# Kernel optimization log

Hardware: AMD Instinct MI355X
Metric: run time of the kernel (lower is better)

## Reference

```python
import jax, jax.numpy as jnp
import numpy as np

NUM_HEADS = 16
HIDDEN = 1024
HEAD_DIM = HIDDEN // NUM_HEADS


def setup_inputs() -> dict:
    key = jax.random.key(0)
    ks = jax.random.split(key, 12)
    B, S, H = 4, 1024, HIDDEN
    s = 1.0 / np.sqrt(H)
    inp = {
        "aspect_hidden": jax.random.normal(ks[0], (B, S, H), jnp.float32),
        "opinion_hidden": jax.random.normal(ks[1], (B, S, H), jnp.float32),
        "attention_mask": jnp.ones((B, S), jnp.int32),
        # torch nn.Linear weights are [out, in]
        "Wq": jax.random.normal(ks[2], (H, H), jnp.float32) * s,
        "bq": jnp.zeros((H,), jnp.float32),
        "Wk": jax.random.normal(ks[3], (H, H), jnp.float32) * s,
        "bk": jnp.zeros((H,), jnp.float32),
        "Wv": jax.random.normal(ks[4], (H, H), jnp.float32) * s,
        "bv": jnp.zeros((H,), jnp.float32),
        "Wo": jax.random.normal(ks[5], (H, H), jnp.float32) * s,
        "bo": jnp.zeros((H,), jnp.float32),
        # nn.Bilinear(H, H, 1): weight [1, H, H], bias [1]
        "Wbil": jax.random.normal(ks[6], (1, H, H), jnp.float32) * s,
        "bbil": jnp.zeros((1,), jnp.float32),
    }
    return inp


def reference(aspect_hidden, opinion_hidden, attention_mask,
              Wq, bq, Wk, bk, Wv, bv, Wo, bo, Wbil, bbil):
    B, Sq, H = aspect_hidden.shape
    Sk = opinion_hidden.shape[1]
    nh, hd = NUM_HEADS, HEAD_DIM
    scale = hd ** (-0.5)

    q = (aspect_hidden @ Wq.T + bq).reshape(B, Sq, nh, hd).transpose(0, 2, 1, 3)
    k = (opinion_hidden @ Wk.T + bk).reshape(B, Sk, nh, hd).transpose(0, 2, 1, 3)
    v = (opinion_hidden @ Wv.T + bv).reshape(B, Sk, nh, hd).transpose(0, 2, 1, 3)

    # bilinear span bias: span[b,s] = a[b,s] @ Wbil[0] @ o[b,s] + bbil
    span = jnp.einsum('bsh,hk,bsk->bs', aspect_hidden, Wbil[0], opinion_hidden) + bbil[0]

    # scores [B, nh, Sq, Sk] with span bias broadcast over heads and keys
    scores = jnp.einsum('bhqd,bhkd->bhqk', q, k) * scale + span[:, None, :, None]
    scores = jnp.where(attention_mask[:, None, None, :] == 0, -jnp.inf, scores)

    probs = jax.nn.softmax(scores, axis=-1)
    ctx = jnp.einsum('bhqk,bhkd->bhqd', probs, v)
    ctx = ctx.transpose(0, 2, 1, 3).reshape(B, Sq, H)
    return ctx @ Wo.T + bo
```

## Files before the change

kernel.cpp:

```cpp
#include <hip/hip_runtime.h>
#include <hip/hip_bf16.h>
#include <stdint.h>

typedef __attribute__((ext_vector_type(4))) float f32x4;
typedef __attribute__((ext_vector_type(16))) float f32x16;
typedef __attribute__((ext_vector_type(8))) short bf16x8;
typedef __attribute__((ext_vector_type(4))) unsigned int u32x4;
typedef unsigned short u16;

#define GBL_AS1(p) ((const __attribute__((address_space(1))) void*)(p))
#define LDS_AS3(p) ((__attribute__((address_space(3))) void*)(p))

static __device__ __forceinline__ u16 f2bf(float f) {
  __hip_bfloat16 h = __float2bfloat16(f);
  union { __hip_bfloat16 h; u16 u; } c; c.h = h;
  return c.u;
}

__global__ __launch_bounds__(256) void cast_f32_bf16(const float* __restrict__ src,
                                                     u16* __restrict__ dst, int n4) {
  int i = blockIdx.x * blockDim.x + threadIdx.x;
  if (i >= n4) return;
  float4 v = reinterpret_cast<const float4*>(src)[i];
  ushort4 o;
  o.x = f2bf(v.x); o.y = f2bf(v.y); o.z = f2bf(v.z); o.w = f2bf(v.w);
  reinterpret_cast<ushort4*>(dst)[i] = o;
}

static __device__ __forceinline__ void gemm_core(const u16* __restrict__ Atile,
                                                 const u16* __restrict__ Btile,
                                                 u16* lds_a, u16* lds_b,
                                                 f32x4 acc[4][4]) {
  const int tid = threadIdx.x;
  const int lane = tid & 63;
  const int wv = tid >> 6;
  const int wm = wv >> 1, wn = wv & 1;
  const int fr = lane & 15, fq = lane >> 4;
  for (int kt = 0; kt < 32; ++kt) {
#pragma unroll
    for (int i = 0; i < 2; ++i) {
      const int cb = (wv * 2 + i) * 64;
      const int c = cb + lane;
      const int row = c >> 2;
      const int off = (c & 3) * 8;
      __builtin_amdgcn_global_load_lds(GBL_AS1(Atile + (size_t)row * 1024 + kt * 32 + off),
                                       LDS_AS3(lds_a + cb * 8), 16, 0, 0);
      __builtin_amdgcn_global_load_lds(GBL_AS1(Btile + (size_t)row * 1024 + kt * 32 + off),
                                       LDS_AS3(lds_b + cb * 8), 16, 0, 0);
    }
    __syncthreads();
    bf16x8 af[4], bfv[4];
#pragma unroll
    for (int mi = 0; mi < 4; ++mi)
      af[mi] = *(const bf16x8*)&lds_a[(wm * 64 + mi * 16 + fr) * 32 + fq * 8];
#pragma unroll
    for (int ni = 0; ni < 4; ++ni)
      bfv[ni] = *(const bf16x8*)&lds_b[(wn * 64 + ni * 16 + fr) * 32 + fq * 8];
#pragma unroll
    for (int mi = 0; mi < 4; ++mi)
#pragma unroll
      for (int ni = 0; ni < 4; ++ni)
        acc[mi][ni] = __builtin_amdgcn_mfma_f32_16x16x32_bf16(af[mi], bfv[ni], acc[mi][ni], 0, 0, 0);
    __syncthreads();
  }
}

__global__ __launch_bounds__(256) void qkv_gemm(
    const u16* __restrict__ aB, const u16* __restrict__ oB,
    const u16* __restrict__ Wq, const u16* __restrict__ Wk, const u16* __restrict__ Wv,
    const float* __restrict__ bq, const float* __restrict__ bk, const float* __restrict__ bv,
    u16* __restrict__ q_ws, u16* __restrict__ k_ws, u16* __restrict__ vt_ws) {
  __shared__ __align__(16) u16 lds_a[128 * 32];
  __shared__ __align__(16) u16 lds_b[128 * 32];
  const int mt = blockIdx.x;
  const int nt = blockIdx.y;
  const int w = nt >> 3, ntl = nt & 7;
  const u16* A = (w == 0) ? aB : oB;
  const u16* W = (w == 0) ? Wq : (w == 1) ? Wk : Wv;
  const float* bias = (w == 0) ? bq : (w == 1) ? bk : bv;
  f32x4 acc[4][4];
#pragma unroll
  for (int i = 0; i < 4; ++i)
#pragma unroll
    for (int j = 0; j < 4; ++j) acc[i][j] = (f32x4){0.f, 0.f, 0.f, 0.f};
  gemm_core(A + (size_t)mt * 128 * 1024, W + (size_t)ntl * 128 * 1024, lds_a, lds_b, acc);
  const int lane = threadIdx.x & 63, wvi = threadIdx.x >> 6;
  const int wm = wvi >> 1, wn = wvi & 1, fr = lane & 15, fq = lane >> 4;
  u16* dst01 = (w == 0) ? q_ws : k_ws;
#pragma unroll
  for (int mi = 0; mi < 4; ++mi)
#pragma unroll
    for (int ni = 0; ni < 4; ++ni)
#pragma unroll
      for (int r = 0; r < 4; ++r) {
        int m = mt * 128 + wm * 64 + mi * 16 + fq * 4 + r;
        int nl = ntl * 128 + wn * 64 + ni * 16 + fr;
        float v = acc[mi][ni][r] + bias[nl];
        int b = m >> 10, s = m & 1023, h = nl >> 6, d = nl & 63;
        u16 u = f2bf(v);
        if (w < 2) dst01[(((size_t)(b * 16 + h)) * 1024 + s) * 64 + d] = u;
        else       vt_ws[(((size_t)(b * 16 + h)) * 64 + d) * 1024 + s] = u;
      }
}

__global__ __launch_bounds__(256, 2) void attn_kernel(
    const u16* __restrict__ q_ws, const u16* __restrict__ k_ws,
    const u16* __restrict__ vt_ws, const int* __restrict__ mask,
    u16* __restrict__ ctx_ws) {
  __shared__ __align__(16) u16 k_lds[2][128 * 64];
  __shared__ __align__(16) u16 vt_lds[2][64 * 128];
  __shared__ __align__(16) float mb_lds[2][128];
  __shared__ __align__(16) float scl_lds[4][32];
  const int bid = blockIdx.x;
  const int bh = bid & 63, qt = bid >> 6;
  const int b = bh >> 4, h = bh & 15;
  const int tid = threadIdx.x, lane = tid & 63, wv = tid >> 6;
  const int l31 = lane & 31, hi = lane >> 5;
  const u16* qbase = q_ws + (size_t)bh * 65536 + (size_t)qt * 8192;
  const u16* kbase = k_ws + (size_t)bh * 65536;
  const u16* vtbase = vt_ws + (size_t)bh * 65536;
  const int* maskb = mask + b * 1024;
  const float SCL2 = 0.18033688f;

#define STAGE_KV(kt_, buf_) do { \
    _Pragma("unroll") \
    for (int i_ = 0; i_ < 4; ++i_) { \
      int cb_ = (wv * 4 + i_) * 64; \
      int c_ = cb_ + lane; \
      int rK_ = c_ >> 3, cK_ = c_ & 7; \
      __builtin_amdgcn_global_load_lds(GBL_AS1(kbase + (size_t)((kt_) * 128 + rK_) * 64 + ((cK_ ^ (rK_ & 7)) * 8)), \
                                       LDS_AS3(&k_lds[buf_][cb_ * 8]), 16, 0, 0); \
      int rV_ = c_ >> 4, cV_ = c_ & 15; \
      __builtin_amdgcn_global_load_lds(GBL_AS1(vtbase + (size_t)rV_ * 1024 + (kt_) * 128 + ((cV_ ^ (rV_ & 15)) * 8)), \
                                       LDS_AS3(&vt_lds[buf_][cb_ * 8]), 16, 0, 0); \
    } \
    if (tid < 128) mb_lds[buf_][tid] = maskb[(kt_) * 128 + tid] ? 0.0f : -30000.0f; \
  } while (0)

#pragma unroll
  for (int i_ = 0; i_ < 4; ++i_) {
    int cb_ = (wv * 4 + i_) * 64;
    int c_ = cb_ + lane;
    int rQ = c_ >> 3, cQ = c_ & 7;
    __builtin_amdgcn_global_load_lds(GBL_AS1(qbase + (size_t)rQ * 64 + ((cQ ^ (rQ & 7)) * 8)),
                                     LDS_AS3(&k_lds[1][cb_ * 8]), 16, 0, 0);
  }
  if (tid < 128) mb_lds[0][tid] = maskb[tid] ? 0.0f : -30000.0f;
  __syncthreads();
  bf16x8 qf[4];
  {
    int rq = wv * 32 + l31;
    const u16* qr = &k_lds[1][rq * 64];
    int rx = rq & 7;
#pragma unroll
    for (int ds = 0; ds < 4; ++ds)
      qf[ds] = *(const bf16x8*)&qr[((ds * 2 + hi) ^ rx) * 8];
  }
  __syncthreads();
  STAGE_KV(0, 0);
  __syncthreads();

  f32x16 ctx0, ctx1;
#pragma unroll
  for (int z = 0; z < 16; ++z) { ctx0[z] = 0.f; ctx1[z] = 0.f; }
  float mrow = -1e30f, lrow = 0.f;

  for (int kt = 0; kt < 8; ++kt) {
    const int cur = kt & 1;
    if (kt < 7) STAGE_KV(kt + 1, (kt + 1) & 1);

    f32x16 sc[4];
#pragma unroll
    for (int kb = 0; kb < 4; ++kb) {
      f32x16 a;
#pragma unroll
      for (int z = 0; z < 16; ++z) a[z] = 0.f;
      int r = kb * 32 + l31;
      const u16* kr = &k_lds[cur][r * 64];
      int rx = r & 7;
#pragma unroll
      for (int ds = 0; ds < 4; ++ds) {
        bf16x8 kf = *(const bf16x8*)&kr[((ds * 2 + hi) ^ rx) * 8];
        a = __builtin_amdgcn_mfma_f32_32x32x16_bf16(kf, qf[ds], a, 0, 0, 0);
      }
      sc[kb] = a;
    }

    float pmax = -3.0e38f;
#pragma unroll
    for (int kb = 0; kb < 4; ++kb)
#pragma unroll
      for (int g = 0; g < 4; ++g) {
        float4 mb = *(const float4*)&mb_lds[cur][kb * 32 + g * 8 + hi * 4];
        const float* mbp = (const float*)&mb;
#pragma unroll
        for (int i2 = 0; i2 < 4; ++i2) {
          float v = fmaf(sc[kb][g * 4 + i2], SCL2, mbp[i2]);
          sc[kb][g * 4 + i2] = v;
          pmax = fmaxf(pmax, v);
        }
      }
    pmax = fmaxf(pmax, __shfl_xor(pmax, 32));

    if (__any(pmax > mrow + 8.0f)) {
      float mnew = fmaxf(mrow, pmax);
      float scl = __builtin_exp2f(mrow - mnew);
      mrow = mnew;
      lrow *= scl;
      if (hi == 0) scl_lds[wv][l31] = scl;
      asm volatile("s_waitcnt lgkmcnt(0)" ::: "memory");
#pragma unroll
      for (int g = 0; g < 4; ++g) {
        float4 s4 = *(const float4*)&scl_lds[wv][g * 8 + hi * 4];
        const float* sp = (const float*)&s4;
#pragma unroll
        for (int i2 = 0; i2 < 4; ++i2) {
          ctx0[g * 4 + i2] *= sp[i2];
          ctx1[g * 4 + i2] *= sp[i2];
        }
      }
    }

    float psum = 0.f;
#pragma unroll
    for (int kb = 0; kb < 4; ++kb)
#pragma unroll
      for (int r2 = 0; r2 < 16; ++r2) {
        float p = __builtin_exp2f(sc[kb][r2] - mrow);
        sc[kb][r2] = p;
        psum += p;
      }
    psum += __shfl_xor(psum, 32);
    lrow += psum;

#pragma unroll
    for (int kb = 0; kb < 4; ++kb) {
      unsigned int w[8];
#pragma unroll
      for (int j = 0; j < 8; ++j) {
        unsigned int t;
        asm("v_cvt_pk_bf16_f32 %0, %1, %2" : "=v"(t) : "v"(sc[kb][2 * j]), "v"(sc[kb][2 * j + 1]));
        w[j] = t;
      }
      unsigned int sw0 = (unsigned)__shfl_xor((int)w[0], 32), sw1 = (unsigned)__shfl_xor((int)w[1], 32);
      unsigned int sw2 = (unsigned)__shfl_xor((int)w[2], 32), sw3 = (unsigned)__shfl_xor((int)w[3], 32);
      unsigned int sw4 = (unsigned)__shfl_xor((int)w[4], 32), sw5 = (unsigned)__shfl_xor((int)w[5], 32);
      unsigned int sw6 = (unsigned)__shfl_xor((int)w[6], 32), sw7 = (unsigned)__shfl_xor((int)w[7], 32);
      union { u32x4 u; bf16x8 b; } P0, P1;
      P0.u = (u32x4){ hi ? sw2 : w[0], hi ? sw3 : w[1], hi ? w[2] : sw0, hi ? w[3] : sw1 };
      P1.u = (u32x4){ hi ? sw6 : w[4], hi ? sw7 : w[5], hi ? w[6] : sw4, hi ? w[7] : sw5 };
#pragma unroll
      for (int db = 0; db < 2; ++db) {
        int rv = db * 32 + l31;
        const u16* vr = &vt_lds[cur][rv * 128];
        int rvx = rv & 15;
        bf16x8 v0 = *(const bf16x8*)&vr[((kb * 4 + hi) ^ rvx) * 8];
        bf16x8 v1 = *(const bf16x8*)&vr[((kb * 4 + 2 + hi) ^ rvx) * 8];
        if (db == 0) {
          ctx0 = __builtin_amdgcn_mfma_f32_32x32x16_bf16(P0.b, v0, ctx0, 0, 0, 0);
          ctx0 = __builtin_amdgcn_mfma_f32_32x32x16_bf16(P1.b, v1, ctx0, 0, 0, 0);
        } else {
          ctx1 = __builtin_amdgcn_mfma_f32_32x32x16_bf16(P0.b, v0, ctx1, 0, 0, 0);
          ctx1 = __builtin_amdgcn_mfma_f32_32x32x16_bf16(P1.b, v1, ctx1, 0, 0, 0);
        }
      }
    }
    __syncthreads();
  }

  float inv = (lrow > 0.f) ? 1.0f / lrow : 0.f;
  if (hi == 0) scl_lds[wv][l31] = inv;
  asm volatile("s_waitcnt lgkmcnt(0)" ::: "memory");
  const int sbase = qt * 128 + wv * 32;
#pragma unroll
  for (int g = 0; g < 4; ++g) {
    float4 s4 = *(const float4*)&scl_lds[wv][g * 8 + hi * 4];
    const float* sp = (const float*)&s4;
#pragma unroll
    for (int i2 = 0; i2 < 4; ++i2) {
      int s = sbase + g * 8 + hi * 4 + i2;
      size_t rowoff = ((size_t)(b * 1024 + s)) * 1024 + h * 64;
      ctx_ws[rowoff + l31]      = f2bf(ctx0[g * 4 + i2] * sp[i2]);
      ctx_ws[rowoff + 32 + l31] = f2bf(ctx1[g * 4 + i2] * sp[i2]);
    }
  }
#undef STAGE_KV
}

__global__ __launch_bounds__(256) void out_gemm(const u16* __restrict__ ctxB,
                                                const u16* __restrict__ Wo,
                                                const float* __restrict__ bo,
                                                float* __restrict__ out) {
  __shared__ __align__(16) u16 lds_a[128 * 32];
  __shared__ __align__(16) u16 lds_b[128 * 32];
  const int mt = blockIdx.x, nt = blockIdx.y;
  f32x4 acc[4][4];
#pragma unroll
  for (int i = 0; i < 4; ++i)
#pragma unroll
    for (int j = 0; j < 4; ++j) acc[i][j] = (f32x4){0.f, 0.f, 0.f, 0.f};
  gemm_core(ctxB + (size_t)mt * 128 * 1024, Wo + (size_t)nt * 128 * 1024, lds_a, lds_b, acc);
  const int lane = threadIdx.x & 63, wvi = threadIdx.x >> 6;
  const int wm = wvi >> 1, wn = wvi & 1, fr = lane & 15, fq = lane >> 4;
#pragma unroll
  for (int mi = 0; mi < 4; ++mi)
#pragma unroll
    for (int ni = 0; ni < 4; ++ni)
#pragma unroll
      for (int r = 0; r < 4; ++r) {
        int m = mt * 128 + wm * 64 + mi * 16 + fq * 4 + r;
        int n = nt * 128 + wn * 64 + ni * 16 + fr;
        out[(size_t)m * 1024 + n] = acc[mi][ni][r] + bo[n];
      }
}

extern "C" void kernel_launch(void* const* d_in, const int* in_sizes, int n_in,
                              void* d_out, int out_size, void* d_ws, size_t ws_size,
                              hipStream_t stream) {
  const float* aspect = (const float*)d_in[0];
  const float* opinion = (const float*)d_in[1];
  const int* mask = (const int*)d_in[2];
  const float* Wq = (const float*)d_in[3];
  const float* bq = (const float*)d_in[4];
  const float* Wk = (const float*)d_in[5];
  const float* bk = (const float*)d_in[6];
  const float* Wv = (const float*)d_in[7];
  const float* bv = (const float*)d_in[8];
  const float* Wo = (const float*)d_in[9];
  const float* bo = (const float*)d_in[10];
  float* out = (float*)d_out;
  char* ws = (char*)d_ws;

  const size_t MB = 1u << 20;
  u16* aB    = (u16*)(ws + 0 * MB);
  u16* oB    = (u16*)(ws + 8 * MB);
  u16* WqB   = (u16*)(ws + 16 * MB);
  u16* WkB   = (u16*)(ws + 18 * MB);
  u16* WvB   = (u16*)(ws + 20 * MB);
  u16* WoB   = (u16*)(ws + 22 * MB);
  u16* q_ws  = (u16*)(ws + 24 * MB);
  u16* k_ws  = (u16*)(ws + 32 * MB);
  u16* vt_ws = (u16*)(ws + 40 * MB);
  u16* ctx_ws= (u16*)(ws + 48 * MB);

  cast_f32_bf16<<<4096, 256, 0, stream>>>(aspect, aB, 1048576);
  cast_f32_bf16<<<4096, 256, 0, stream>>>(opinion, oB, 1048576);
  cast_f32_bf16<<<1024, 256, 0, stream>>>(Wq, WqB, 262144);
  cast_f32_bf16<<<1024, 256, 0, stream>>>(Wk, WkB, 262144);
  cast_f32_bf16<<<1024, 256, 0, stream>>>(Wv, WvB, 262144);
  cast_f32_bf16<<<1024, 256, 0, stream>>>(Wo, WoB, 262144);
  qkv_gemm<<<dim3(32, 24), 256, 0, stream>>>(aB, oB, WqB, WkB, WvB, bq, bk, bv,
                                             q_ws, k_ws, vt_ws);
  attn_kernel<<<512, 256, 0, stream>>>(q_ws, k_ws, vt_ws, mask, ctx_ws);
  out_gemm<<<dim3(32, 8), 256, 0, stream>>>(ctx_ws, WoB, bo, out);
}
```

Before: 124.0 us.

## Fuse casts, double-buffer swizzled GEMMs, shrink attention key tiles, precompute mask flags

Replaces the six cast launches with one fused cast kernel, which also records per-64-key mask flags. The shared GEMM core moves to K=64 tiles with XOR-swizzled LDS and double buffering, so global loads overlap the MFMA work. The softmax scale is folded into Q at the QKV epilogue. Attention now uses 64-key tiles with smaller LDS to allow occupancy 4, and applies the mask only in tiles whose flag is set. The flags live in the tail of the output buffer, which out_gemm later overwrites; this relies on out_size being an element count and on kernel ordering.

```diff
diff --git a/kernel.cpp b/kernel.cpp
--- a/kernel.cpp
+++ b/kernel.cpp
@@ -17,61 +17,100 @@
   return c.u;
 }
 
-__global__ __launch_bounds__(256) void cast_f32_bf16(const float* __restrict__ src,
-                                                     u16* __restrict__ dst, int n4) {
-  int i = blockIdx.x * blockDim.x + threadIdx.x;
-  if (i >= n4) return;
-  float4 v = reinterpret_cast<const float4*>(src)[i];
-  ushort4 o;
-  o.x = f2bf(v.x); o.y = f2bf(v.y); o.z = f2bf(v.z); o.w = f2bf(v.w);
-  reinterpret_cast<ushort4*>(dst)[i] = o;
-}
-
-static __device__ __forceinline__ void gemm_core(const u16* __restrict__ Atile,
-                                                 const u16* __restrict__ Btile,
-                                                 u16* lds_a, u16* lds_b,
-                                                 f32x4 acc[4][4]) {
-  const int tid = threadIdx.x;
-  const int lane = tid & 63;
-  const int wv = tid >> 6;
+__global__ __launch_bounds__(256) void fused_cast(
+    const float* __restrict__ a, const float* __restrict__ o,
+    const float* __restrict__ wq_, const float* __restrict__ wk_,
+    const float* __restrict__ wv_, const float* __restrict__ wo_,
+    const int* __restrict__ mask,
+    u16* __restrict__ aB, u16* __restrict__ oB,
+    u16* __restrict__ WqB, u16* __restrict__ WkB,
+    u16* __restrict__ WvB, u16* __restrict__ WoB,
+    int* __restrict__ flags) {
+  if (blockIdx.x == 0 && threadIdx.x < 64) {
+    int bb = threadIdx.x >> 4, kt = threadIdx.x & 15;
+    int anyz = 0;
+    for (int s = 0; s < 64; ++s) anyz |= (mask[bb * 1024 + kt * 64 + s] == 0);
+    flags[threadIdx.x] = anyz;
+  }
+  int idx = blockIdx.x * 256 + threadIdx.x;
+#pragma unroll
+  for (int j = 0; j < 4; ++j) {
+    int i = idx + j * 786432;
+    const float* src; u16* dst; int off;
+    if (i < 1048576) { src = a; dst = aB; off = i; }
+    else if (i < 2097152) { src = o; dst = oB; off = i - 1048576; }
+    else {
+      int w = (i - 2097152) >> 18; off = (i - 2097152) & 262143;
+      src = (w == 0) ? wq_ : (w == 1) ? wk_ : (w == 2) ? wv_ : wo_;
+      dst = (w == 0) ? WqB : (w == 1) ? WkB : (w == 2) ? WvB : WoB;
+    }
+    float4 v = reinterpret_cast<const float4*>(src)[off];
+    ushort4 ov;
+    ov.x = f2bf(v.x); ov.y = f2bf(v.y); ov.z = f2bf(v.z); ov.w = f2bf(v.w);
+    reinterpret_cast<ushort4*>(dst)[off] = ov;
+  }
+}
+
+static __device__ __forceinline__ void gemm_core2(const u16* __restrict__ A,
+                                                  const u16* __restrict__ B,
+                                                  u16* lds_a, u16* lds_b,
+                                                  f32x4 acc[4][4]) {
+  const int tid = threadIdx.x, lane = tid & 63, wv = tid >> 6;
   const int wm = wv >> 1, wn = wv & 1;
   const int fr = lane & 15, fq = lane >> 4;
-  for (int kt = 0; kt < 32; ++kt) {
-#pragma unroll
-    for (int i = 0; i < 2; ++i) {
-      const int cb = (wv * 2 + i) * 64;
-      const int c = cb + lane;
-      const int row = c >> 2;
-      const int off = (c & 3) * 8;
-      __builtin_amdgcn_global_load_lds(GBL_AS1(Atile + (size_t)row * 1024 + kt * 32 + off),
-                                       LDS_AS3(lds_a + cb * 8), 16, 0, 0);
-      __builtin_amdgcn_global_load_lds(GBL_AS1(Btile + (size_t)row * 1024 + kt * 32 + off),
-                                       LDS_AS3(lds_b + cb * 8), 16, 0, 0);
+
+#define GSTAGE(kt_, buf_) do { \
+    _Pragma("unroll") \
+    for (int i_ = 0; i_ < 4; ++i_) { \
+      int cb_ = (wv * 4 + i_) * 64; \
+      int c_ = cb_ + lane; \
+      int r_ = c_ >> 3; \
+      int sc_ = ((c_ & 7) ^ (r_ & 7)) * 8; \
+      __builtin_amdgcn_global_load_lds(GBL_AS1(A + (size_t)r_ * 1024 + (kt_) * 64 + sc_), \
+                                       LDS_AS3(lds_a + (buf_) * 8192 + cb_ * 8), 16, 0, 0); \
+      __builtin_amdgcn_global_load_lds(GBL_AS1(B + (size_t)r_ * 1024 + (kt_) * 64 + sc_), \
+                                       LDS_AS3(lds_b + (buf_) * 8192 + cb_ * 8), 16, 0, 0); \
+    } \
+  } while (0)
+
+  GSTAGE(0, 0);
+  __syncthreads();
+  for (int kt = 0; kt < 16; ++kt) {
+    const int cur = kt & 1;
+    if (kt < 15) GSTAGE(kt + 1, cur ^ 1);
+    const u16* la = lds_a + cur * 8192;
+    const u16* lb = lds_b + cur * 8192;
+#pragma unroll
+    for (int ks = 0; ks < 2; ++ks) {
+      bf16x8 af[4], bfv[4];
+#pragma unroll
+      for (int mi = 0; mi < 4; ++mi) {
+        int r = wm * 64 + mi * 16 + fr;
+        af[mi] = *(const bf16x8*)&la[r * 64 + (((ks * 4 + fq) ^ (r & 7)) * 8)];
+      }
+#pragma unroll
+      for (int ni = 0; ni < 4; ++ni) {
+        int r = wn * 64 + ni * 16 + fr;
+        bfv[ni] = *(const bf16x8*)&lb[r * 64 + (((ks * 4 + fq) ^ (r & 7)) * 8)];
+      }
+#pragma unroll
+      for (int mi = 0; mi < 4; ++mi)
+#pragma unroll
+        for (int ni = 0; ni < 4; ++ni)
+          acc[mi][ni] = __builtin_amdgcn_mfma_f32_16x16x32_bf16(af[mi], bfv[ni], acc[mi][ni], 0, 0, 0);
     }
     __syncthreads();
-    bf16x8 af[4], bfv[4];
-#pragma unroll
-    for (int mi = 0; mi < 4; ++mi)
-      af[mi] = *(const bf16x8*)&lds_a[(wm * 64 + mi * 16 + fr) * 32 + fq * 8];
-#pragma unroll
-    for (int ni = 0; ni < 4; ++ni)
-      bfv[ni] = *(const bf16x8*)&lds_b[(wn * 64 + ni * 16 + fr) * 32 + fq * 8];
-#pragma unroll
-    for (int mi = 0; mi < 4; ++mi)
-#pragma unroll
-      for (int ni = 0; ni < 4; ++ni)
-        acc[mi][ni] = __builtin_amdgcn_mfma_f32_16x16x32_bf16(af[mi], bfv[ni], acc[mi][ni], 0, 0, 0);
-    __syncthreads();
-  }
-}
-
-__global__ __launch_bounds__(256) void qkv_gemm(
+  }
+#undef GSTAGE
+}
+
+__global__ __launch_bounds__(256, 2) void qkv_gemm(
     const u16* __restrict__ aB, const u16* __restrict__ oB,
     const u16* __restrict__ Wq, const u16* __restrict__ Wk, const u16* __restrict__ Wv,
     const float* __restrict__ bq, const float* __restrict__ bk, const float* __restrict__ bv,
     u16* __restrict__ q_ws, u16* __restrict__ k_ws, u16* __restrict__ vt_ws) {
-  __shared__ __align__(16) u16 lds_a[128 * 32];
-  __shared__ __align__(16) u16 lds_b[128 * 32];
+  __shared__ __align__(16) u16 lds_a[2 * 128 * 64];
+  __shared__ __align__(16) u16 lds_b[2 * 128 * 64];
   const int mt = blockIdx.x;
   const int nt = blockIdx.y;
   const int w = nt >> 3, ntl = nt & 7;
@@ -83,10 +122,11 @@
   for (int i = 0; i < 4; ++i)
 #pragma unroll
     for (int j = 0; j < 4; ++j) acc[i][j] = (f32x4){0.f, 0.f, 0.f, 0.f};
-  gemm_core(A + (size_t)mt * 128 * 1024, W + (size_t)ntl * 128 * 1024, lds_a, lds_b, acc);
+  gemm_core2(A + (size_t)mt * 128 * 1024, W + (size_t)ntl * 128 * 1024, lds_a, lds_b, acc);
   const int lane = threadIdx.x & 63, wvi = threadIdx.x >> 6;
   const int wm = wvi >> 1, wn = wvi & 1, fr = lane & 15, fq = lane >> 4;
   u16* dst01 = (w == 0) ? q_ws : k_ws;
+  const float qscl = (w == 0) ? 0.18033688f : 1.0f;
 #pragma unroll
   for (int mi = 0; mi < 4; ++mi)
 #pragma unroll
@@ -95,7 +135,7 @@
       for (int r = 0; r < 4; ++r) {
         int m = mt * 128 + wm * 64 + mi * 16 + fq * 4 + r;
         int nl = ntl * 128 + wn * 64 + ni * 16 + fr;
-        float v = acc[mi][ni][r] + bias[nl];
+        float v = (acc[mi][ni][r] + bias[nl]) * qscl;
         int b = m >> 10, s = m & 1023, h = nl >> 6, d = nl & 63;
         u16 u = f2bf(v);
         if (w < 2) dst01[(((size_t)(b * 16 + h)) * 1024 + s) * 64 + d] = u;
@@ -103,13 +143,12 @@
       }
 }
 
-__global__ __launch_bounds__(256, 2) void attn_kernel(
+__global__ __launch_bounds__(256, 4) void attn_kernel(
     const u16* __restrict__ q_ws, const u16* __restrict__ k_ws,
     const u16* __restrict__ vt_ws, const int* __restrict__ mask,
-    u16* __restrict__ ctx_ws) {
-  __shared__ __align__(16) u16 k_lds[2][128 * 64];
-  __shared__ __align__(16) u16 vt_lds[2][64 * 128];
-  __shared__ __align__(16) float mb_lds[2][128];
+    const int* __restrict__ flags, u16* __restrict__ ctx_ws) {
+  __shared__ __align__(16) u16 k_lds[2][64 * 64];
+  __shared__ __align__(16) u16 vt_lds[2][64 * 64];
   __shared__ __align__(16) float scl_lds[4][32];
   const int bid = blockIdx.x;
   const int bh = bid & 63, qt = bid >> 6;
@@ -119,38 +158,38 @@
   const u16* qbase = q_ws + (size_t)bh * 65536 + (size_t)qt * 8192;
   const u16* kbase = k_ws + (size_t)bh * 65536;
   const u16* vtbase = vt_ws + (size_t)bh * 65536;
-  const int* maskb = mask + b * 1024;
-  const float SCL2 = 0.18033688f;
 
 #define STAGE_KV(kt_, buf_) do { \
     _Pragma("unroll") \
-    for (int i_ = 0; i_ < 4; ++i_) { \
-      int cb_ = (wv * 4 + i_) * 64; \
+    for (int i_ = 0; i_ < 2; ++i_) { \
+      int cb_ = (wv * 2 + i_) * 64; \
       int c_ = cb_ + lane; \
-      int rK_ = c_ >> 3, cK_ = c_ & 7; \
-      __builtin_amdgcn_global_load_lds(GBL_AS1(kbase + (size_t)((kt_) * 128 + rK_) * 64 + ((cK_ ^ (rK_ & 7)) * 8)), \
+      int r_ = c_ >> 3; \
+      int sc_ = ((c_ & 7) ^ (r_ & 7)) * 8; \
+      __builtin_amdgcn_global_load_lds(GBL_AS1(kbase + (size_t)((kt_) * 64 + r_) * 64 + sc_), \
                                        LDS_AS3(&k_lds[buf_][cb_ * 8]), 16, 0, 0); \
-      int rV_ = c_ >> 4, cV_ = c_ & 15; \
-      __builtin_amdgcn_global_load_lds(GBL_AS1(vtbase + (size_t)rV_ * 1024 + (kt_) * 128 + ((cV_ ^ (rV_ & 15)) * 8)), \
+      __builtin_amdgcn_global_load_lds(GBL_AS1(vtbase + (size_t)r_ * 1024 + (kt_) * 64 + sc_), \
                                        LDS_AS3(&vt_lds[buf_][cb_ * 8]), 16, 0, 0); \
     } \
-    if (tid < 128) mb_lds[buf_][tid] = maskb[(kt_) * 128 + tid] ? 0.0f : -30000.0f; \
   } while (0)
 
-#pragma unroll
-  for (int i_ = 0; i_ < 4; ++i_) {
-    int cb_ = (wv * 4 + i_) * 64;
-    int c_ = cb_ + lane;
-    int rQ = c_ >> 3, cQ = c_ & 7;
-    __builtin_amdgcn_global_load_lds(GBL_AS1(qbase + (size_t)rQ * 64 + ((cQ ^ (rQ & 7)) * 8)),
-                                     LDS_AS3(&k_lds[1][cb_ * 8]), 16, 0, 0);
-  }
-  if (tid < 128) mb_lds[0][tid] = maskb[tid] ? 0.0f : -30000.0f;
+  {
+    u16* qstage = &k_lds[0][0];
+#pragma unroll
+    for (int i_ = 0; i_ < 4; ++i_) {
+      int cb_ = (wv * 4 + i_) * 64;
+      int c_ = cb_ + lane;
+      int r_ = c_ >> 3;
+      int sc_ = ((c_ & 7) ^ (r_ & 7)) * 8;
+      __builtin_amdgcn_global_load_lds(GBL_AS1(qbase + (size_t)r_ * 64 + sc_),
+                                       LDS_AS3(qstage + cb_ * 8), 16, 0, 0);
+    }
+  }
   __syncthreads();
   bf16x8 qf[4];
   {
     int rq = wv * 32 + l31;
-    const u16* qr = &k_lds[1][rq * 64];
+    const u16* qr = &k_lds[0][0] + rq * 64;
     int rx = rq & 7;
 #pragma unroll
     for (int ds = 0; ds < 4; ++ds)
@@ -165,13 +204,13 @@
   for (int z = 0; z < 16; ++z) { ctx0[z] = 0.f; ctx1[z] = 0.f; }
   float mrow = -1e30f, lrow = 0.f;
 
-  for (int kt = 0; kt < 8; ++kt) {
+  for (int kt = 0; kt < 16; ++kt) {
     const int cur = kt & 1;
-    if (kt < 7) STAGE_KV(kt + 1, (kt + 1) & 1);
-
-    f32x16 sc[4];
-#pragma unroll
-    for (int kb = 0; kb < 4; ++kb) {
+    if (kt < 15) STAGE_KV(kt + 1, cur ^ 1);
+
+    f32x16 sc[2];
+#pragma unroll
+    for (int kb = 0; kb < 2; ++kb) {
       f32x16 a;
 #pragma unroll
       for (int z = 0; z < 16; ++z) a[z] = 0.f;
@@ -186,20 +225,21 @@
       sc[kb] = a;
     }
 
+    if (flags[b * 16 + kt]) {
+#pragma unroll
+      for (int kb = 0; kb < 2; ++kb)
+#pragma unroll
+        for (int r2 = 0; r2 < 16; ++r2) {
+          int key = kb * 32 + (r2 & 3) + 8 * (r2 >> 2) + 4 * hi;
+          if (mask[b * 1024 + kt * 64 + key] == 0) sc[kb][r2] = -30000.0f;
+        }
+    }
+
     float pmax = -3.0e38f;
 #pragma unroll
-    for (int kb = 0; kb < 4; ++kb)
-#pragma unroll
-      for (int g = 0; g < 4; ++g) {
-        float4 mb = *(const float4*)&mb_lds[cur][kb * 32 + g * 8 + hi * 4];
-        const float* mbp = (const float*)&mb;
-#pragma unroll
-        for (int i2 = 0; i2 < 4; ++i2) {
-          float v = fmaf(sc[kb][g * 4 + i2], SCL2, mbp[i2]);
-          sc[kb][g * 4 + i2] = v;
-          pmax = fmaxf(pmax, v);
-        }
-      }
+    for (int kb = 0; kb < 2; ++kb)
+#pragma unroll
+      for (int r2 = 0; r2 < 16; ++r2) pmax = fmaxf(pmax, sc[kb][r2]);
     pmax = fmaxf(pmax, __shfl_xor(pmax, 32));
 
     if (__any(pmax > mrow + 8.0f)) {
@@ -223,7 +263,7 @@
 
     float psum = 0.f;
 #pragma unroll
-    for (int kb = 0; kb < 4; ++kb)
+    for (int kb = 0; kb < 2; ++kb)
 #pragma unroll
       for (int r2 = 0; r2 < 16; ++r2) {
         float p = __builtin_exp2f(sc[kb][r2] - mrow);
@@ -234,7 +274,7 @@
     lrow += psum;
 
 #pragma unroll
-    for (int kb = 0; kb < 4; ++kb) {
+    for (int kb = 0; kb < 2; ++kb) {
       unsigned int w[8];
 #pragma unroll
       for (int j = 0; j < 8; ++j) {
@@ -252,8 +292,8 @@
 #pragma unroll
       for (int db = 0; db < 2; ++db) {
         int rv = db * 32 + l31;
-        const u16* vr = &vt_lds[cur][rv * 128];
-        int rvx = rv & 15;
+        const u16* vr = &vt_lds[cur][rv * 64];
+        int rvx = rv & 7;
         bf16x8 v0 = *(const bf16x8*)&vr[((kb * 4 + hi) ^ rvx) * 8];
         bf16x8 v1 = *(const bf16x8*)&vr[((kb * 4 + 2 + hi) ^ rvx) * 8];
         if (db == 0) {
@@ -287,19 +327,19 @@
 #undef STAGE_KV
 }
 
-__global__ __launch_bounds__(256) void out_gemm(const u16* __restrict__ ctxB,
-                                                const u16* __restrict__ Wo,
-                                                const float* __restrict__ bo,
-                                                float* __restrict__ out) {
-  __shared__ __align__(16) u16 lds_a[128 * 32];
-  __shared__ __align__(16) u16 lds_b[128 * 32];
+__global__ __launch_bounds__(256, 2) void out_gemm(const u16* __restrict__ ctxB,
+                                                   const u16* __restrict__ Wo,
+                                                   const float* __restrict__ bo,
+                                                   float* __restrict__ out) {
+  __shared__ __align__(16) u16 lds_a[2 * 128 * 64];
+  __shared__ __align__(16) u16 lds_b[2 * 128 * 64];
   const int mt = blockIdx.x, nt = blockIdx.y;
   f32x4 acc[4][4];
 #pragma unroll
   for (int i = 0; i < 4; ++i)
 #pragma unroll
     for (int j = 0; j < 4; ++j) acc[i][j] = (f32x4){0.f, 0.f, 0.f, 0.f};
-  gemm_core(ctxB + (size_t)mt * 128 * 1024, Wo + (size_t)nt * 128 * 1024, lds_a, lds_b, acc);
+  gemm_core2(ctxB + (size_t)mt * 128 * 1024, Wo + (size_t)nt * 128 * 1024, lds_a, lds_b, acc);
   const int lane = threadIdx.x & 63, wvi = threadIdx.x >> 6;
   const int wm = wvi >> 1, wn = wvi & 1, fr = lane & 15, fq = lane >> 4;
 #pragma unroll
@@ -342,15 +382,12 @@
   u16* k_ws  = (u16*)(ws + 32 * MB);
   u16* vt_ws = (u16*)(ws + 40 * MB);
   u16* ctx_ws= (u16*)(ws + 48 * MB);
-
-  cast_f32_bf16<<<4096, 256, 0, stream>>>(aspect, aB, 1048576);
-  cast_f32_bf16<<<4096, 256, 0, stream>>>(opinion, oB, 1048576);
-  cast_f32_bf16<<<1024, 256, 0, stream>>>(Wq, WqB, 262144);
-  cast_f32_bf16<<<1024, 256, 0, stream>>>(Wk, WkB, 262144);
-  cast_f32_bf16<<<1024, 256, 0, stream>>>(Wv, WvB, 262144);
-  cast_f32_bf16<<<1024, 256, 0, stream>>>(Wo, WoB, 262144);
+  int* flags = (int*)(out + out_size - 64);
+
+  fused_cast<<<3072, 256, 0, stream>>>(aspect, opinion, Wq, Wk, Wv, Wo, mask,
+                                       aB, oB, WqB, WkB, WvB, WoB, flags);
   qkv_gemm<<<dim3(32, 24), 256, 0, stream>>>(aB, oB, WqB, WkB, WvB, bq, bk, bv,
                                              q_ws, k_ws, vt_ws);
-  attn_kernel<<<512, 256, 0, stream>>>(q_ws, k_ws, vt_ws, mask, ctx_ws);
+  attn_kernel<<<512, 256, 0, stream>>>(q_ws, k_ws, vt_ws, mask, flags, ctx_ws);
   out_gemm<<<dim3(32, 8), 256, 0, stream>>>(ctx_ws, WoB, bo, out);
 }
```

New measurement: 120.3 us. 1.03x faster.
